# Kernel tuning notes

Hardware: AMD Instinct MI355X
Metric: run time of the kernel (lower is better)

Reference implementation:

```python
import jax, jax.numpy as jnp
import numpy as np


def _conv_same(x, w):
    # NHWC input, HWIO kernel, stride 1, SAME padding
    return jax.lax.conv_general_dilated(
        x, w, window_strides=(1, 1), padding='SAME',
        dimension_numbers=('NHWC', 'HWIO', 'NHWC'))


def _maxpool2(x):
    return jax.lax.reduce_window(
        x, -jnp.inf, jax.lax.max,
        window_dimensions=(1, 2, 2, 1), window_strides=(1, 2, 2, 1),
        padding='VALID')


def _binarize(x):
    # sign binarization with straight-through estimator (XNOR-net / Riptide)
    return x + jax.lax.stop_gradient(jnp.sign(x) - x)


def _binary_conv_relu(x, w):
    # BinaryConv2D: binarize activations and weights, conv, relu, no bias
    return jax.nn.relu(_conv_same(_binarize(x), _binarize(w)))


def setup_inputs() -> dict:
    key = jax.random.key(0)
    ks = jax.random.split(key, 32)
    d = {}
    d['x'] = jax.random.normal(ks[0], (128, 32, 32, 3), dtype=jnp.float32)
    d['w1'] = jax.random.normal(ks[1], (3, 3, 3, 128), dtype=jnp.float32) * 0.1
    d['b1'] = jax.random.normal(ks[2], (128,), dtype=jnp.float32) * 0.1
    chans = [128, 128, 256, 256, 512, 512]
    kshapes = [(3, 3, 128, 128), (3, 3, 128, 256), (3, 3, 256, 256),
               (3, 3, 256, 512), (3, 3, 512, 512)]
    for i, shp in zip(range(2, 7), kshapes):
        d[f'w{i}'] = jax.random.normal(ks[2 + i], shp, dtype=jnp.float32) * 0.1
    for i in range(1, 7):
        c = chans[i - 1]
        d[f'bn{i}_scale'] = jax.random.uniform(ks[10 + i], (c,), dtype=jnp.float32, minval=0.5, maxval=1.5)
        d[f'bn{i}_bias'] = jax.random.normal(ks[20 + i], (c,), dtype=jnp.float32) * 0.1
    d['dense_w'] = jax.random.normal(ks[30], (512, 10), dtype=jnp.float32) * 0.05
    d['dense_b'] = jax.random.normal(ks[31], (10,), dtype=jnp.float32) * 0.05
    return d


def reference(x, w1, b1, bn1_scale, bn1_bias, w2, bn2_scale, bn2_bias,
              w3, bn3_scale, bn3_bias, w4, bn4_scale, bn4_bias,
              w5, bn5_scale, bn5_bias, w6, bn6_scale, bn6_bias,
              dense_w, dense_b):
    # conv1: normal float conv + relu, then BN (inference: fused scale/bias)
    h = jax.nn.relu(_conv_same(x, w1) + b1)
    h = h * bn1_scale + bn1_bias
    # conv2 (binary) -> pool -> bn2
    h = _binary_conv_relu(h, w2)
    h = _maxpool2(h)
    h = h * bn2_scale + bn2_bias
    # conv3 (binary) -> bn3
    h = _binary_conv_relu(h, w3)
    h = h * bn3_scale + bn3_bias
    # conv4 (binary) -> pool -> bn4
    h = _binary_conv_relu(h, w4)
    h = _maxpool2(h)
    h = h * bn4_scale + bn4_bias
    # conv5 (binary) -> bn5
    h = _binary_conv_relu(h, w5)
    h = h * bn5_scale + bn5_bias
    # conv6 (binary) -> pool -> bn6
    h = _binary_conv_relu(h, w6)
    h = _maxpool2(h)  # -> [B, 4, 4, 512]
    h = h * bn6_scale + bn6_bias
    # Dense applied on last axis (original code has no flatten): [B,4,4,10]
    logits = jnp.einsum('bhwc,cd->bhwd', h, dense_w) + dense_b
    return jax.nn.softmax(logits, axis=-1)
```

## Files before the change

kernel.cpp:

```cpp
#include <hip/hip_runtime.h>
#include <cstdint>
#include <math.h>

typedef unsigned long long u64;


__global__ void zero_kernel(u64* __restrict__ p, int n) {
    int i = blockIdx.x * blockDim.x + threadIdx.x;
    int stride = gridDim.x * blockDim.x;
    for (; i < n; i += stride) p[i] = 0;
}

__global__ __launch_bounds__(256) void pack_kernel(
        const float* __restrict__ w2, const float* __restrict__ w3,
        const float* __restrict__ w4, const float* __restrict__ w5,
        const float* __restrict__ w6,
        u64* __restrict__ wq2, u64* __restrict__ wq3, u64* __restrict__ wq4,
        u64* __restrict__ wq5, u64* __restrict__ wq6) {
    int wid = (blockIdx.x * 256 + threadIdx.x) >> 6;
    int lane = threadIdx.x & 63;
    const float* w; u64* wq; int Wi, Cout, base;
    if      (wid <  2304) { w = w2; wq = wq2; Wi = 2; Cout = 128; base = 0; }
    else if (wid <  6912) { w = w3; wq = wq3; Wi = 2; Cout = 256; base = 2304; }
    else if (wid < 16128) { w = w4; wq = wq4; Wi = 4; Cout = 256; base = 6912; }
    else if (wid < 34560) { w = w5; wq = wq5; Wi = 4; Cout = 512; base = 16128; }
    else if (wid < 71424) { w = w6; wq = wq6; Wi = 8; Cout = 512; base = 34560; }
    else return;
    int id = wid - base;
    int oc = id % Cout;
    int tw = id / Cout;
    int tap = tw / Wi, cw = tw % Wi;
    int Cin = Wi * 64;
    float v = w[((size_t)tap * Cin + cw * 64 + lane) * Cout + oc];
    u64 mask = __ballot(!(v > 0.0f));
    if (lane == 0) wq[((size_t)oc * Wi + cw) * 9 + tap] = mask;
}

__global__ __launch_bounds__(256) void meta_kernel(
        const u64* __restrict__ wq2, const u64* __restrict__ wq3,
        const u64* __restrict__ wq4, const u64* __restrict__ wq5,
        const u64* __restrict__ wq6,
        const float* s2, const float* b2, const float* s3, const float* b3,
        const float* s4, const float* b4, const float* s5, const float* b5,
        const float* s6, const float* b6,
        int* __restrict__ mt) {
    int wid = (blockIdx.x * 256 + threadIdx.x) >> 6;
    int lane = threadIdx.x & 63;
    if (wid >= 1664) return;
    const u64* wq; int WI, oc, mbase; const float* sc; const float* bi;
    if      (wid <  128) { wq = wq2; WI = 2; oc = wid;        mbase = 0;     sc = s2; bi = b2; }
    else if (wid <  384) { wq = wq3; WI = 2; oc = wid - 128;  mbase = 1536;  sc = s3; bi = b3; }
    else if (wid <  640) { wq = wq4; WI = 4; oc = wid - 384;  mbase = 4608;  sc = s4; bi = b4; }
    else if (wid < 1152) { wq = wq5; WI = 4; oc = wid - 640;  mbase = 7680;  sc = s5; bi = b5; }
    else                 { wq = wq6; WI = 8; oc = wid - 1152; mbase = 13824; sc = s6; bi = b6; }
    int P = 0;
    if (lane < 9) {
        int s = 0;
        for (int cw = 0; cw < WI; cw++)
            s += (int)__popcll(wq[((size_t)oc * WI + cw) * 9 + lane]);
        P = 64 * WI - s;
    }
    int p0 = __shfl(P, 0, 64), p1 = __shfl(P, 1, 64), p2 = __shfl(P, 2, 64);
    int p3 = __shfl(P, 3, 64), p5 = __shfl(P, 5, 64);
    int p6 = __shfl(P, 6, 64), p7 = __shfl(P, 7, 64), p8 = __shfl(P, 8, 64);
    if (lane == 0) {
        int* mo = mt + mbase + oc * 12;
        mo[0] = p0 + p1 + p2;
        mo[1] = p6 + p7 + p8;
        mo[2] = p0 + p3 + p6;
        mo[3] = p2 + p5 + p8;
        mo[4] = p0; mo[5] = p2; mo[6] = p6; mo[7] = p8;
        double tneg = -(double)bi[oc] / (double)sc[oc];
        mo[8] = (tneg < 0.0) ? -(1 << 29) : (int)floor(tneg);
    }
}

__global__ __launch_bounds__(128) void conv1_pack_kernel(
        const float* __restrict__ x, const float* __restrict__ w1,
        const float* __restrict__ b1, const float* __restrict__ s1,
        const float* __restrict__ bb1, u64* __restrict__ p1) {
    const int t = threadIdx.x;
    const int oc = t;
    const int bx = blockIdx.x;
    const int xseg = (bx & 3) << 3;
    const int y = (bx >> 2) & 31;
    const int b = bx >> 7;

    double wreg[27];
    #pragma unroll
    for (int k = 0; k < 27; k++) wreg[k] = (double)w1[k * 128 + oc];
    const double b1v = (double)b1[oc];
    const double tneg = -(double)bb1[oc] / (double)s1[oc];
    const bool always = tneg < 0.0;
    const double thr = tneg - b1v;

    double acc[8];
    #pragma unroll
    for (int i = 0; i < 8; i++) acc[i] = 0.0;

    #pragma unroll
    for (int ky = 0; ky < 3; ky++) {
        int iy = y - 1 + ky;
        if (iy < 0 || iy > 31) continue;
        #pragma unroll
        for (int col = 0; col < 10; col++) {
            int ix = xseg - 1 + col;
            if (ix < 0 || ix > 31) continue;
            const float* xp = x + ((b * 32 + iy) * 32 + ix) * 3;
            #pragma unroll
            for (int c = 0; c < 3; c++) {
                double xv = (double)xp[c];
                #pragma unroll
                for (int kx = 0; kx < 3; kx++) {
                    int px = col - kx;
                    if (px >= 0 && px < 8)
                        acc[px] += xv * wreg[(ky * 3 + kx) * 3 + c];
                }
            }
        }
    }
    const int w = t >> 6;
    #pragma unroll
    for (int px = 0; px < 8; px++) {
        bool bit = always || (acc[px] > thr);
        u64 m = __ballot(bit);
        if ((t & 63) == 0)
            p1[(((size_t)w * 128 + b) * 34 + y + 1) * 34 + xseg + px + 1] = m;
    }
}

template<int WI, int H, int W, int COUT, bool POOL, bool BITOUT>
__global__ __launch_bounds__(256, 4) void bconv61_kernel(
        const u64* __restrict__ in, const u64* __restrict__ wq,
        const int* __restrict__ mt,
        const float* __restrict__ bns, const float* __restrict__ bnb,
        u64* __restrict__ outb, float* __restrict__ outf) {
    constexpr int OCG = 8;
    constexpr int Hp = H + 2, Wp = W + 2;
    constexpr int Ho = POOL ? H / 2 : H;
    constexpr int Wo = POOL ? W / 2 : W;
    constexpr int TX = W / 8;
    constexpr int TILES = (H / 8) * (W / 8);
    constexpr int NG = COUT / OCG;

    const int lane = threadIdx.x & 63;
    int wid = (blockIdx.x * blockDim.x + threadIdx.x) >> 6;
    wid = __builtin_amdgcn_readfirstlane(wid);
    const int g = wid % NG;
    int tb = wid / NG;
    const int tile = tb % TILES;
    const int b = tb / TILES;
    if (b >= 128) return;
    const int ly = lane >> 3, lx = lane & 7;
    const int py = (tile / TX) * 8 + ly;
    const int px = (tile % TX) * 8 + lx;
    const int oc0 = g * OCG;

    const int ft = (py == 0), fb = (py == H - 1);
    const int fl = (px == 0), fr = (px == W - 1);
    const int ctl = ft & fl, ctr = ft & fr, cbl = fb & fl, cbr = fb & fr;
    const int n_oob = 3 * (ft + fb + fl + fr) - ctl - ctr - cbl - cbr;
    const int dbase = -64 * WI * (9 + n_oob);
    const bool anyedge = __ballot(ft | fb | fl | fr) != 0;

    int m[OCG];
    #pragma unroll
    for (int o = 0; o < OCG; o++) m[o] = 0;

    const u64* ab = in + ((size_t)b * Hp + py) * Wp + px;
    const u64* wb0 = wq + (size_t)oc0 * WI * 9;

    #pragma unroll 1
    for (int cw = 0; cw < WI; cw++) {
        const u64* ap = ab + (size_t)cw * (128 * Hp * Wp);
        u64 act[9];
        #pragma unroll
        for (int ky = 0; ky < 3; ky++)
            #pragma unroll
            for (int kx = 0; kx < 3; kx++)
                act[ky * 3 + kx] = ap[ky * Wp + kx];
        const u64* wb = wb0 + (size_t)cw * 9;
        #pragma unroll
        for (int o = 0; o < OCG; o++) {
            const u64* wl = wb + (size_t)o * (WI * 9);
            int a0 = m[o], a1 = 0, a2 = 0, a3 = 0;
            #pragma unroll
            for (int t9 = 0; t9 < 9; t9++) {
                u64 xo = act[t9] ^ wl[t9];
                int lo = __builtin_popcount((unsigned)xo);
                int hi = __builtin_popcount((unsigned)(xo >> 32));
                if (t9 & 1) { a1 = lo + a1; a3 = hi + a3; }
                else        { a0 = lo + a0; a2 = hi + a2; }
            }
            m[o] = (a0 + a2) + (a1 + a3);
        }
    }

    const bool master = POOL ? (((ly | lx) & 1) == 0) : true;
    const int opy = POOL ? (py >> 1) : py, opx = POOL ? (px >> 1) : px;
    unsigned mask = 0;

    #pragma unroll
    for (int o = 0; o < OCG; o++) {
        const int* mo = mt + (size_t)(oc0 + o) * 12;
        int d;
        if (anyedge) {
            int S = ft * mo[0] + fb * mo[1] + fl * mo[2] + fr * mo[3]
                  - ctl * mo[4] - ctr * mo[5] - cbl * mo[6] - cbr * mo[7];
            d = 2 * (m[o] + S) + dbase;
        } else {
            d = 2 * m[o] - 64 * WI * 9;
        }
        if constexpr (BITOUT) {
            mask |= (unsigned)(d > mo[8]) << o;
        } else {
            int dm = max(d, __shfl_xor(d, 1, 64));
            int dp = max(dm, __shfl_xor(dm, 8, 64));
            int pmax = dp > 0 ? dp : 0;
            float h = (float)pmax * bns[oc0 + o] + bnb[oc0 + o];
            if (master)
                outf[(size_t)((b * 4 + opy) * 4 + opx) * 512 + oc0 + o] = h;
        }
    }

    if constexpr (BITOUT) {
        if constexpr (POOL) {
            mask |= __shfl_xor(mask, 1, 64);
            mask |= __shfl_xor(mask, 8, 64);
        }
        if (master) {
            size_t idx = (((size_t)(oc0 >> 6) * 128 + b) * (Ho + 2) + opy + 1)
                         * (Wo + 2) + opx + 1;
            char* bp = (char*)(outb + idx) + ((oc0 & 63) >> 3);
            *(unsigned char*)bp = (unsigned char)mask;
        }
    }
}

__global__ __launch_bounds__(256) void dense_softmax_kernel(
        const float* __restrict__ h6, const float* __restrict__ dw,
        const float* __restrict__ db, float* __restrict__ out) {
    int lane = threadIdx.x & 63;
    int r = (blockIdx.x * blockDim.x + threadIdx.x) >> 6;
    if (r >= 2048) return;
    const float* hr = h6 + (size_t)r * 512;
    float part[10];
    #pragma unroll
    for (int d = 0; d < 10; d++) part[d] = 0.f;
    #pragma unroll
    for (int k = 0; k < 8; k++) {
        int c = lane + 64 * k;
        float hv = hr[c];
        const float* dwr = dw + c * 10;
        #pragma unroll
        for (int d = 0; d < 10; d++) part[d] += hv * dwr[d];
    }
    #pragma unroll
    for (int off = 32; off >= 1; off >>= 1) {
        #pragma unroll
        for (int d = 0; d < 10; d++) part[d] += __shfl_down(part[d], off, 64);
    }
    if (lane == 0) {
        float logits[10];
        float mx = -1e30f;
        #pragma unroll
        for (int d = 0; d < 10; d++) { logits[d] = part[d] + db[d]; mx = fmaxf(mx, logits[d]); }
        float se = 0.f;
        #pragma unroll
        for (int d = 0; d < 10; d++) { logits[d] = expf(logits[d] - mx); se += logits[d]; }
        float inv = 1.f / se;
        #pragma unroll
        for (int d = 0; d < 10; d++) out[(size_t)r * 10 + d] = logits[d] * inv;
    }
}

extern "C" void kernel_launch(void* const* d_in, const int* in_sizes, int n_in,
                              void* d_out, int out_size, void* d_ws, size_t ws_size,
                              hipStream_t stream) {
    const float* x    = (const float*)d_in[0];
    const float* w1   = (const float*)d_in[1];
    const float* b1   = (const float*)d_in[2];
    const float* w2   = (const float*)d_in[3];
    const float* w3   = (const float*)d_in[4];
    const float* w4   = (const float*)d_in[5];
    const float* w5   = (const float*)d_in[6];
    const float* w6   = (const float*)d_in[7];
    const float* bn1s = (const float*)d_in[8];
    const float* bn1b = (const float*)d_in[9];
    const float* bn2s = (const float*)d_in[10];
    const float* bn2b = (const float*)d_in[11];
    const float* bn3s = (const float*)d_in[12];
    const float* bn3b = (const float*)d_in[13];
    const float* bn4s = (const float*)d_in[14];
    const float* bn4b = (const float*)d_in[15];
    const float* bn5s = (const float*)d_in[16];
    const float* bn5b = (const float*)d_in[17];
    const float* bn6s = (const float*)d_in[18];
    const float* bn6b = (const float*)d_in[19];
    const float* dw   = (const float*)d_in[20];
    const float* db   = (const float*)d_in[21];
    float* out = (float*)d_out;

    u64* ws   = (u64*)d_ws;
    u64* wq2  = ws;
    u64* wq3  = ws + 2304;
    u64* wq4  = ws + 6912;
    u64* wq5  = ws + 16128;
    u64* wq6  = ws + 34560;
    int* mt   = (int*)(ws + 71424);
    u64* p1   = ws + 81408;
    u64* p2   = ws + 377344;
    u64* p3   = ws + 460288;
    u64* p4   = ws + 626176;
    u64* p5   = ws + 677376;
    float* h6 = (float*)(ws + 779776);
    const int NPAD = 295936 + 82944 + 165888 + 51200 + 102400;

    int* mt2 = mt + 0;
    int* mt3 = mt + 1536;
    int* mt4 = mt + 4608;
    int* mt5 = mt + 7680;
    int* mt6 = mt + 13824;

    zero_kernel<<<1024, 256, 0, stream>>>(p1, NPAD);
    pack_kernel<<<17856, 256, 0, stream>>>(w2, w3, w4, w5, w6,
                                           wq2, wq3, wq4, wq5, wq6);
    meta_kernel<<<416, 256, 0, stream>>>(wq2, wq3, wq4, wq5, wq6,
        bn2s, bn2b, bn3s, bn3b, bn4s, bn4b, bn5s, bn5b, bn6s, bn6b, mt);

    conv1_pack_kernel<<<128*32*4, 128, 0, stream>>>(x, w1, b1, bn1s, bn1b, p1);

    bconv61_kernel<2,32,32,128,true, true ><<<8192, 256, 0, stream>>>(p1, wq2, mt2, nullptr, nullptr, p2, nullptr);
    bconv61_kernel<2,16,16,256,false,true ><<<4096, 256, 0, stream>>>(p2, wq3, mt3, nullptr, nullptr, p3, nullptr);
    bconv61_kernel<4,16,16,256,true, true ><<<4096, 256, 0, stream>>>(p3, wq4, mt4, nullptr, nullptr, p4, nullptr);
    bconv61_kernel<4,8,8,  512,false,true ><<<2048, 256, 0, stream>>>(p4, wq5, mt5, nullptr, nullptr, p5, nullptr);
    bconv61_kernel<8,8,8,  512,true, false><<<2048, 256, 0, stream>>>(p5, wq6, mt6, bn6s, bn6b, nullptr, h6);

    dense_softmax_kernel<<<512, 256, 0, stream>>>(h6, dw, db, out);
}
```

Measured before the change: 332.5 us.

## Fuse zero/pack/meta prep into one kernel and use bcnt accumulate in bconv

```diff
diff --git a/kernel.cpp b/kernel.cpp
--- a/kernel.cpp
+++ b/kernel.cpp
@@ -5,73 +5,78 @@
 typedef unsigned long long u64;
 
 
-__global__ void zero_kernel(u64* __restrict__ p, int n) {
-    int i = blockIdx.x * blockDim.x + threadIdx.x;
-    int stride = gridDim.x * blockDim.x;
-    for (; i < n; i += stride) p[i] = 0;
-}
-
-__global__ __launch_bounds__(256) void pack_kernel(
+__device__ __forceinline__ int bcnt2(u64 x, int acc) {
+    int r;
+    asm("v_bcnt_u32_b32 %0, %1, %3\n\t"
+        "v_bcnt_u32_b32 %0, %2, %0"
+        : "=&v"(r)
+        : "v"((unsigned)x), "v"((unsigned)(x >> 32)), "v"(acc));
+    return r;
+}
+
+__global__ __launch_bounds__(256) void prep_kernel(
         const float* __restrict__ w2, const float* __restrict__ w3,
         const float* __restrict__ w4, const float* __restrict__ w5,
         const float* __restrict__ w6,
         u64* __restrict__ wq2, u64* __restrict__ wq3, u64* __restrict__ wq4,
-        u64* __restrict__ wq5, u64* __restrict__ wq6) {
-    int wid = (blockIdx.x * 256 + threadIdx.x) >> 6;
-    int lane = threadIdx.x & 63;
-    const float* w; u64* wq; int Wi, Cout, base;
-    if      (wid <  2304) { w = w2; wq = wq2; Wi = 2; Cout = 128; base = 0; }
-    else if (wid <  6912) { w = w3; wq = wq3; Wi = 2; Cout = 256; base = 2304; }
-    else if (wid < 16128) { w = w4; wq = wq4; Wi = 4; Cout = 256; base = 6912; }
-    else if (wid < 34560) { w = w5; wq = wq5; Wi = 4; Cout = 512; base = 16128; }
-    else if (wid < 71424) { w = w6; wq = wq6; Wi = 8; Cout = 512; base = 34560; }
-    else return;
-    int id = wid - base;
-    int oc = id % Cout;
-    int tw = id / Cout;
-    int tap = tw / Wi, cw = tw % Wi;
-    int Cin = Wi * 64;
-    float v = w[((size_t)tap * Cin + cw * 64 + lane) * Cout + oc];
-    u64 mask = __ballot(!(v > 0.0f));
-    if (lane == 0) wq[((size_t)oc * Wi + cw) * 9 + tap] = mask;
-}
-
-__global__ __launch_bounds__(256) void meta_kernel(
-        const u64* __restrict__ wq2, const u64* __restrict__ wq3,
-        const u64* __restrict__ wq4, const u64* __restrict__ wq5,
-        const u64* __restrict__ wq6,
+        u64* __restrict__ wq5, u64* __restrict__ wq6,
         const float* s2, const float* b2, const float* s3, const float* b3,
         const float* s4, const float* b4, const float* s5, const float* b5,
         const float* s6, const float* b6,
-        int* __restrict__ mt) {
-    int wid = (blockIdx.x * 256 + threadIdx.x) >> 6;
+        int* __restrict__ mt, u64* __restrict__ pz, int nz) {
+    const int ZB = 1024;
+    if (blockIdx.x < ZB) {
+        int i = blockIdx.x * 256 + threadIdx.x;
+        const int stride = ZB * 256;
+        for (; i < nz; i += stride) pz[i] = 0;
+        return;
+    }
+    int wid = ((blockIdx.x - ZB) * 256 + threadIdx.x) >> 6;
     int lane = threadIdx.x & 63;
-    if (wid >= 1664) return;
-    const u64* wq; int WI, oc, mbase; const float* sc; const float* bi;
-    if      (wid <  128) { wq = wq2; WI = 2; oc = wid;        mbase = 0;     sc = s2; bi = b2; }
-    else if (wid <  384) { wq = wq3; WI = 2; oc = wid - 128;  mbase = 1536;  sc = s3; bi = b3; }
-    else if (wid <  640) { wq = wq4; WI = 4; oc = wid - 384;  mbase = 4608;  sc = s4; bi = b4; }
-    else if (wid < 1152) { wq = wq5; WI = 4; oc = wid - 640;  mbase = 7680;  sc = s5; bi = b5; }
-    else                 { wq = wq6; WI = 8; oc = wid - 1152; mbase = 13824; sc = s6; bi = b6; }
-    int P = 0;
-    if (lane < 9) {
-        int s = 0;
-        for (int cw = 0; cw < WI; cw++)
-            s += (int)__popcll(wq[((size_t)oc * WI + cw) * 9 + lane]);
-        P = 64 * WI - s;
-    }
-    int p0 = __shfl(P, 0, 64), p1 = __shfl(P, 1, 64), p2 = __shfl(P, 2, 64);
-    int p3 = __shfl(P, 3, 64), p5 = __shfl(P, 5, 64);
-    int p6 = __shfl(P, 6, 64), p7 = __shfl(P, 7, 64), p8 = __shfl(P, 8, 64);
-    if (lane == 0) {
-        int* mo = mt + mbase + oc * 12;
-        mo[0] = p0 + p1 + p2;
-        mo[1] = p6 + p7 + p8;
-        mo[2] = p0 + p3 + p6;
-        mo[3] = p2 + p5 + p8;
-        mo[4] = p0; mo[5] = p2; mo[6] = p6; mo[7] = p8;
-        double tneg = -(double)bi[oc] / (double)sc[oc];
-        mo[8] = (tneg < 0.0) ? -(1 << 29) : (int)floor(tneg);
+    if (wid < 71424) {
+        const float* w; u64* wq; int Wi, Cout, base;
+        if      (wid <  2304) { w = w2; wq = wq2; Wi = 2; Cout = 128; base = 0; }
+        else if (wid <  6912) { w = w3; wq = wq3; Wi = 2; Cout = 256; base = 2304; }
+        else if (wid < 16128) { w = w4; wq = wq4; Wi = 4; Cout = 256; base = 6912; }
+        else if (wid < 34560) { w = w5; wq = wq5; Wi = 4; Cout = 512; base = 16128; }
+        else                  { w = w6; wq = wq6; Wi = 8; Cout = 512; base = 34560; }
+        int id = wid - base;
+        int oc = id % Cout;
+        int tw = id / Cout;
+        int tap = tw / Wi, cw = tw % Wi;
+        int Cin = Wi * 64;
+        float v = w[((size_t)tap * Cin + cw * 64 + lane) * Cout + oc];
+        u64 mask = __ballot(!(v > 0.0f));
+        if (lane == 0) wq[((size_t)oc * Wi + cw) * 9 + tap] = mask;
+    } else if (wid < 71424 + 1664) {
+        int id2 = wid - 71424;
+        const float* w; const float* sc; const float* bi; int Wi, Cout, oc, mbase;
+        if      (id2 <  128) { w = w2; Wi = 2; Cout = 128; oc = id2;        mbase = 0;     sc = s2; bi = b2; }
+        else if (id2 <  384) { w = w3; Wi = 2; Cout = 256; oc = id2 - 128;  mbase = 1536;  sc = s3; bi = b3; }
+        else if (id2 <  640) { w = w4; Wi = 4; Cout = 256; oc = id2 - 384;  mbase = 4608;  sc = s4; bi = b4; }
+        else if (id2 < 1152) { w = w5; Wi = 4; Cout = 512; oc = id2 - 640;  mbase = 7680;  sc = s5; bi = b5; }
+        else                 { w = w6; Wi = 8; Cout = 512; oc = id2 - 1152; mbase = 13824; sc = s6; bi = b6; }
+        int Cin = Wi * 64;
+        int P[9];
+        #pragma unroll
+        for (int tap = 0; tap < 9; tap++) {
+            int cnt = 0;
+            for (int cw = 0; cw < Wi; cw++) {
+                float v = w[((size_t)tap * Cin + cw * 64 + lane) * Cout + oc];
+                cnt += (int)__popcll(__ballot(v > 0.0f));
+            }
+            P[tap] = cnt;
+        }
+        if (lane == 0) {
+            int* mo = mt + mbase + oc * 12;
+            mo[0] = P[0] + P[1] + P[2];
+            mo[1] = P[6] + P[7] + P[8];
+            mo[2] = P[0] + P[3] + P[6];
+            mo[3] = P[2] + P[5] + P[8];
+            mo[4] = P[0]; mo[5] = P[2]; mo[6] = P[6]; mo[7] = P[8];
+            double tneg = -(double)bi[oc] / (double)sc[oc];
+            mo[8] = (tneg < 0.0) ? -(1 << 29) : (int)floor(tneg);
+        }
     }
 }
 
@@ -130,7 +135,7 @@
 }
 
 template<int WI, int H, int W, int COUT, bool POOL, bool BITOUT>
-__global__ __launch_bounds__(256, 4) void bconv61_kernel(
+__global__ __launch_bounds__(256, 4) void bconv62_kernel(
         const u64* __restrict__ in, const u64* __restrict__ wq,
         const int* __restrict__ mt,
         const float* __restrict__ bns, const float* __restrict__ bnb,
@@ -183,16 +188,11 @@
         #pragma unroll
         for (int o = 0; o < OCG; o++) {
             const u64* wl = wb + (size_t)o * (WI * 9);
-            int a0 = m[o], a1 = 0, a2 = 0, a3 = 0;
+            int acc = m[o];
             #pragma unroll
-            for (int t9 = 0; t9 < 9; t9++) {
-                u64 xo = act[t9] ^ wl[t9];
-                int lo = __builtin_popcount((unsigned)xo);
-                int hi = __builtin_popcount((unsigned)(xo >> 32));
-                if (t9 & 1) { a1 = lo + a1; a3 = hi + a3; }
-                else        { a0 = lo + a0; a2 = hi + a2; }
-            }
-            m[o] = (a0 + a2) + (a1 + a3);
+            for (int t9 = 0; t9 < 9; t9++)
+                acc = bcnt2(act[t9] ^ wl[t9], acc);
+            m[o] = acc;
         }
     }
 
@@ -322,19 +322,18 @@
     int* mt5 = mt + 7680;
     int* mt6 = mt + 13824;
 
-    zero_kernel<<<1024, 256, 0, stream>>>(p1, NPAD);
-    pack_kernel<<<17856, 256, 0, stream>>>(w2, w3, w4, w5, w6,
-                                           wq2, wq3, wq4, wq5, wq6);
-    meta_kernel<<<416, 256, 0, stream>>>(wq2, wq3, wq4, wq5, wq6,
-        bn2s, bn2b, bn3s, bn3b, bn4s, bn4b, bn5s, bn5b, bn6s, bn6b, mt);
+    prep_kernel<<<1024 + 18272, 256, 0, stream>>>(
+        w2, w3, w4, w5, w6, wq2, wq3, wq4, wq5, wq6,
+        bn2s, bn2b, bn3s, bn3b, bn4s, bn4b, bn5s, bn5b, bn6s, bn6b,
+        mt, p1, NPAD);
 
     conv1_pack_kernel<<<128*32*4, 128, 0, stream>>>(x, w1, b1, bn1s, bn1b, p1);
 
-    bconv61_kernel<2,32,32,128,true, true ><<<8192, 256, 0, stream>>>(p1, wq2, mt2, nullptr, nullptr, p2, nullptr);
-    bconv61_kernel<2,16,16,256,false,true ><<<4096, 256, 0, stream>>>(p2, wq3, mt3, nullptr, nullptr, p3, nullptr);
-    bconv61_kernel<4,16,16,256,true, true ><<<4096, 256, 0, stream>>>(p3, wq4, mt4, nullptr, nullptr, p4, nullptr);
-    bconv61_kernel<4,8,8,  512,false,true ><<<2048, 256, 0, stream>>>(p4, wq5, mt5, nullptr, nullptr, p5, nullptr);
-    bconv61_kernel<8,8,8,  512,true, false><<<2048, 256, 0, stream>>>(p5, wq6, mt6, bn6s, bn6b, nullptr, h6);
+    bconv62_kernel<2,32,32,128,true, true ><<<8192, 256, 0, stream>>>(p1, wq2, mt2, nullptr, nullptr, p2, nullptr);
+    bconv62_kernel<2,16,16,256,false,true ><<<4096, 256, 0, stream>>>(p2, wq3, mt3, nullptr, nullptr, p3, nullptr);
+    bconv62_kernel<4,16,16,256,true, true ><<<4096, 256, 0, stream>>>(p3, wq4, mt4, nullptr, nullptr, p4, nullptr);
+    bconv62_kernel<4,8,8,  512,false,true ><<<2048, 256, 0, stream>>>(p4, wq5, mt5, nullptr, nullptr, p5, nullptr);
+    bconv62_kernel<8,8,8,  512,true, false><<<2048, 256, 0, stream>>>(p5, wq6, mt6, bn6s, bn6b, nullptr, h6);
 
     dense_softmax_kernel<<<512, 256, 0, stream>>>(h6, dw, db, out);
 }
```

Measured after the change: 363.1 us. +9.2%, slower.
